# Performance work log

Measured on AMD Instinct MI355X. Metric: run time of the kernel, lower is better.

## Reference

```python
import jax, jax.numpy as jnp
import numpy as np

B, T = 128, 2048
O, E, L = 128, 512, 34  # o_size, embed_dim, num_letter


def setup_inputs() -> dict:
    key = jax.random.key(0)
    ks = jax.random.split(key, 16)
    u = lambda k, shape, s: jax.random.uniform(k, shape, jnp.float32, -s, s)
    hk = jax.random.normal(ks[0], (B, T, O), jnp.float32)
    hv = jax.random.normal(ks[1], (B, T, O), jnp.float32)
    y_1 = jax.random.normal(ks[2], (B, E), jnp.float32)
    c_1 = jax.random.normal(ks[3], (B, O), jnp.float32)
    sh_1 = jax.random.normal(ks[4], (B, O), jnp.float32)
    sc_1 = jax.random.normal(ks[5], (B, O), jnp.float32)
    # valid-length mask (each row has at least T//2 valid positions)
    lengths = jax.random.randint(ks[6], (B,), T // 2, T + 1)
    mask = (jnp.arange(T)[None, :] < lengths[:, None]).astype(jnp.float32)
    s_rnn = 1.0 / np.sqrt(O)
    W_ih = u(ks[7], (4 * O, O + E), s_rnn)
    b_ih = u(ks[8], (4 * O,), s_rnn)
    W_hh = u(ks[9], (4 * O, O), s_rnn)
    b_hh = u(ks[10], (4 * O,), s_rnn)
    s1 = 1.0 / np.sqrt(O)
    W1 = u(ks[11], (L, O), s1); b1 = u(ks[12], (L,), s1)
    W2 = u(ks[13], (L, O), s1); b2 = u(ks[14], (L,), s1)
    s3 = 1.0 / np.sqrt(L)
    W3 = u(ks[15], (L, L), s3); b3 = u(jax.random.fold_in(key, 99), (L,), s3)
    return {"hk": hk, "hv": hv, "y_1": y_1, "c_1": c_1, "sh_1": sh_1,
            "sc_1": sc_1, "mask": mask, "W_ih": W_ih, "b_ih": b_ih,
            "W_hh": W_hh, "b_hh": b_hh, "W1": W1, "b1": b1,
            "W2": W2, "b2": b2, "W3": W3, "b3": b3}


def reference(hk, hv, y_1, c_1, sh_1, sc_1, mask,
              W_ih, b_ih, W_hh, b_hh, W1, b1, W2, b2, W3, b3):
    # LSTMCell (PyTorch gate order: i, f, g, o)
    x = jnp.concatenate([y_1, c_1], axis=1)            # [B, O+E]
    gates = x @ W_ih.T + b_ih + sh_1 @ W_hh.T + b_hh   # [B, 4O]
    i, f, g, o = jnp.split(gates, 4, axis=1)
    sc = jax.nn.sigmoid(f) * sc_1 + jax.nn.sigmoid(i) * jnp.tanh(g)
    sh = jax.nn.sigmoid(o) * jnp.tanh(sc)
    # attention scores keyed on cell state sc (faithful to source)
    scores = jnp.einsum('bto,bo->bt', hk, sc)          # [B, T]
    attn = jax.nn.softmax(scores, axis=1) * mask
    attn = attn / jnp.sum(attn, axis=1, keepdims=True)
    c = jnp.einsum('bt,bto->bo', attn, hv)             # [B, O]
    out = jax.nn.relu(sh @ W1.T + b1 + c @ W2.T + b2)
    out = jax.nn.softmax(out @ W3.T + b3, axis=1)      # [B, L]
    return (out, c, sh, sc)
```

## Files before the change

kernel.cpp:

```cpp
#include <hip/hip_runtime.h>
#include <math.h>

#define BB 128
#define TT 2048
#define OO 128
#define EE 512
#define LL 34
#define XDIM 640
#define CHUNKS 16
#define CHUNK_LEN 128

__device__ __forceinline__ float sigmoidf_(float x) { return 1.0f / (1.0f + __expf(-x)); }

__global__ __launch_bounds__(256) void lstm_kernel(
    const float* __restrict__ y1, const float* __restrict__ c1,
    const float* __restrict__ sh1, const float* __restrict__ sc1,
    const float* __restrict__ Wih, const float* __restrict__ bih,
    const float* __restrict__ Whh, const float* __restrict__ bhh,
    float* __restrict__ out_sh, float* __restrict__ out_sc)
{
    __shared__ float xs[4][768];
    __shared__ float gbuf[4][4][16];
    const int tid = threadIdx.x;
    const int otile = blockIdx.x;
    const int qb = blockIdx.y * 4;

    for (int idx = tid; idx < 4 * 768; idx += 256) {
        int bi = idx / 768, k = idx - bi * 768;
        int b = qb + bi;
        float v;
        if (k < 512)      v = y1[b * EE + k];
        else if (k < 640) v = c1[b * OO + (k - 512)];
        else              v = sh1[b * OO + (k - 640)];
        xs[bi][k] = v;
    }
    __syncthreads();

    const int g = tid >> 6, l = tid & 63;
    #pragma unroll 2
    for (int i = 0; i < 16; ++i) {
        const int row = g * 128 + otile * 16 + i;
        const float* wr = Wih + (size_t)row * XDIM;
        float a0 = 0.f, a1 = 0.f, a2 = 0.f, a3 = 0.f;
        #pragma unroll
        for (int j = 0; j < 10; ++j) {
            float wv = wr[l + 64 * j];
            a0 += wv * xs[0][l + 64 * j];
            a1 += wv * xs[1][l + 64 * j];
            a2 += wv * xs[2][l + 64 * j];
            a3 += wv * xs[3][l + 64 * j];
        }
        const float* wh = Whh + (size_t)row * OO;
        #pragma unroll
        for (int j = 0; j < 2; ++j) {
            float wv = wh[l + 64 * j];
            a0 += wv * xs[0][640 + l + 64 * j];
            a1 += wv * xs[1][640 + l + 64 * j];
            a2 += wv * xs[2][640 + l + 64 * j];
            a3 += wv * xs[3][640 + l + 64 * j];
        }
        #pragma unroll
        for (int off = 32; off >= 1; off >>= 1) {
            a0 += __shfl_xor(a0, off);
            a1 += __shfl_xor(a1, off);
            a2 += __shfl_xor(a2, off);
            a3 += __shfl_xor(a3, off);
        }
        if (l == 0) {
            float bb = bih[row] + bhh[row];
            gbuf[g][0][i] = a0 + bb;
            gbuf[g][1][i] = a1 + bb;
            gbuf[g][2][i] = a2 + bb;
            gbuf[g][3][i] = a3 + bb;
        }
    }
    __syncthreads();

    if (tid < 64) {
        const int bi = tid >> 4, ol = tid & 15;
        const int b = qb + bi, o = otile * 16 + ol;
        float gi = gbuf[0][bi][ol], gf = gbuf[1][bi][ol];
        float gg = gbuf[2][bi][ol], go = gbuf[3][bi][ol];
        float sc = sigmoidf_(gf) * sc1[b * OO + o] + sigmoidf_(gi) * tanhf(gg);
        float sh = sigmoidf_(go) * tanhf(sc);
        out_sc[b * OO + o] = sc;
        out_sh[b * OO + o] = sh;
    }
}

__global__ __launch_bounds__(256) void scores_kernel(
    const float* __restrict__ hk, const float* __restrict__ mask,
    const float* __restrict__ sc, float* __restrict__ wbuf,
    float2* __restrict__ pbuf)
{
    const int b = blockIdx.y, chunk = blockIdx.x;
    const int tid = threadIdx.x;
    const int sg = tid >> 4, l = tid & 15;

    const float4 scA = *(const float4*)(sc + b * OO + l * 8);
    const float4 scB = *(const float4*)(sc + b * OO + l * 8 + 4);

    const int r0 = chunk * CHUNK_LEN + sg * 8;
    const float* mrow = mask + (size_t)b * TT + r0;
    const float* krow = hk + ((size_t)b * TT + r0) * OO;

    float s[8];
    bool val[8];
    #pragma unroll
    for (int i = 0; i < 8; ++i) {
        val[i] = (mrow[i] != 0.f);
        float4 a = make_float4(0.f, 0.f, 0.f, 0.f);
        float4 c2 = make_float4(0.f, 0.f, 0.f, 0.f);
        if (val[i]) {
            a  = *(const float4*)(krow + (size_t)i * OO + l * 8);
            c2 = *(const float4*)(krow + (size_t)i * OO + l * 8 + 4);
        }
        s[i] = a.x * scA.x + a.y * scA.y + a.z * scA.z + a.w * scA.w
             + c2.x * scB.x + c2.y * scB.y + c2.z * scB.z + c2.w * scB.w;
    }
    #pragma unroll
    for (int i = 0; i < 8; ++i) {
        s[i] += __shfl_xor(s[i], 8);
        s[i] += __shfl_xor(s[i], 4);
        s[i] += __shfl_xor(s[i], 2);
        s[i] += __shfl_xor(s[i], 1);
    }
    float msg = -INFINITY;
    #pragma unroll
    for (int i = 0; i < 8; ++i) if (val[i]) msg = fmaxf(msg, s[i]);

    __shared__ float sm[16], ssum[16];
    if (l == 0) sm[sg] = msg;
    __syncthreads();
    float mc = sm[0];
    #pragma unroll
    for (int i = 1; i < 16; ++i) mc = fmaxf(mc, sm[i]);

    float psum = 0.f;
    float e[8];
    #pragma unroll
    for (int i = 0; i < 8; ++i) {
        e[i] = val[i] ? __expf(s[i] - mc) : 0.f;
        psum += e[i];
    }
    if (l == 0) ssum[sg] = psum;
    float* wrow = wbuf + (size_t)b * TT + r0;
    #pragma unroll
    for (int i = 0; i < 8; ++i)
        if (l == i) wrow[i] = e[i];
    __syncthreads();
    if (tid == 0) {
        float S = 0.f;
        #pragma unroll
        for (int i = 0; i < 16; ++i) S += ssum[i];
        pbuf[(size_t)b * CHUNKS + chunk] = make_float2(mc, S);
    }
}

__global__ __launch_bounds__(256) void wsum_kernel(
    const float* __restrict__ hv, const float* __restrict__ wbuf,
    const float2* __restrict__ pbuf, float* __restrict__ ws_c)
{
    const int b = blockIdx.y, chunk = blockIdx.x;
    const int tid = threadIdx.x;
    __shared__ float marr[CHUNKS], Sarr[CHUNKS];
    __shared__ float wsh[CHUNK_LEN];
    __shared__ float pacc[8][128];

    if (tid < CHUNKS) {
        float2 p = pbuf[(size_t)b * CHUNKS + tid];
        marr[tid] = p.x;
        Sarr[tid] = p.y;
    }
    __syncthreads();
    float M = marr[0];
    #pragma unroll
    for (int i = 1; i < CHUNKS; ++i) M = fmaxf(M, marr[i]);
    float S = 0.f;
    #pragma unroll
    for (int i = 0; i < CHUNKS; ++i) S += Sarr[i] * __expf(marr[i] - M);
    const float factor = __expf(marr[chunk] - M) / S;

    if (tid < CHUNK_LEN)
        wsh[tid] = wbuf[(size_t)b * TT + chunk * CHUNK_LEN + tid] * factor;
    __syncthreads();

    const int o4 = tid & 31, rr = tid >> 5;
    const float* vbase = hv + ((size_t)b * TT + chunk * CHUNK_LEN) * OO + o4 * 4;
    float4 acc = make_float4(0.f, 0.f, 0.f, 0.f);
    #pragma unroll 8
    for (int j = 0; j < 16; ++j) {
        const int r = rr + 8 * j;
        const float wr = wsh[r];
        if (wr != 0.f) {
            float4 v = *(const float4*)(vbase + (size_t)r * OO);
            acc.x += wr * v.x;
            acc.y += wr * v.y;
            acc.z += wr * v.z;
            acc.w += wr * v.w;
        }
    }
    *(float4*)&pacc[rr][o4 * 4] = acc;
    __syncthreads();

    if (tid < 128) {
        float s = 0.f;
        #pragma unroll
        for (int i = 0; i < 8; ++i) s += pacc[i][tid];
        ws_c[((size_t)b * CHUNKS + chunk) * OO + tid] = s;
    }
}

__global__ __launch_bounds__(256) void final_kernel(
    const float* __restrict__ ws_c, const float* __restrict__ sh_in,
    const float* __restrict__ W1, const float* __restrict__ b1,
    const float* __restrict__ W2, const float* __restrict__ b2,
    const float* __restrict__ W3, const float* __restrict__ b3,
    float* __restrict__ out_p, float* __restrict__ out_c)
{
    const int b = blockIdx.x, tid = threadIdx.x;
    __shared__ float cbuf[128], shbuf[128], h1[LL], zz[LL], red2[2];

    if (tid < 128) {
        float s = 0.f;
        const float* base = ws_c + (size_t)b * CHUNKS * OO + tid;
        #pragma unroll
        for (int i = 0; i < CHUNKS; ++i) s += base[i * OO];
        cbuf[tid] = s;
        out_c[b * OO + tid] = s;
        shbuf[tid] = sh_in[b * OO + tid];
    }
    __syncthreads();

    const int o = tid >> 2, l2 = tid & 3;
    if (o < LL) {
        float a = 0.f;
        const float* w1r = W1 + o * OO;
        const float* w2r = W2 + o * OO;
        #pragma unroll 8
        for (int j = 0; j < 32; ++j) {
            int k = l2 + 4 * j;
            a += w1r[k] * shbuf[k] + w2r[k] * cbuf[k];
        }
        a += __shfl_xor(a, 1);
        a += __shfl_xor(a, 2);
        if (l2 == 0) h1[o] = fmaxf(a + b1[o] + b2[o], 0.f);
    }
    __syncthreads();

    if (o < LL) {
        float z = 0.f;
        const float* w3r = W3 + o * LL;
        for (int j = 0; j < 9; ++j) {
            int k = l2 + 4 * j;
            if (k < LL) z += w3r[k] * h1[k];
        }
        z += __shfl_xor(z, 1);
        z += __shfl_xor(z, 2);
        if (l2 == 0) zz[o] = z + b3[o];
    }
    __syncthreads();
    if (tid == 0) {
        float mm = zz[0];
        for (int i = 1; i < LL; i++) mm = fmaxf(mm, zz[i]);
        float ss = 0.f;
        for (int i = 0; i < LL; i++) ss += __expf(zz[i] - mm);
        red2[0] = mm; red2[1] = ss;
    }
    __syncthreads();
    if (tid < LL) out_p[b * LL + tid] = __expf(zz[tid] - red2[0]) / red2[1];
}

extern "C" void kernel_launch(void* const* d_in, const int* in_sizes, int n_in,
                              void* d_out, int out_size, void* d_ws, size_t ws_size,
                              hipStream_t stream) {
    (void)in_sizes; (void)n_in; (void)out_size; (void)ws_size;
    const float* hk   = (const float*)d_in[0];
    const float* hv   = (const float*)d_in[1];
    const float* y1   = (const float*)d_in[2];
    const float* c1   = (const float*)d_in[3];
    const float* sh1  = (const float*)d_in[4];
    const float* sc1  = (const float*)d_in[5];
    const float* mask = (const float*)d_in[6];
    const float* Wih  = (const float*)d_in[7];
    const float* bih  = (const float*)d_in[8];
    const float* Whh  = (const float*)d_in[9];
    const float* bhh  = (const float*)d_in[10];
    const float* W1   = (const float*)d_in[11];
    const float* b1   = (const float*)d_in[12];
    const float* W2   = (const float*)d_in[13];
    const float* b2   = (const float*)d_in[14];
    const float* W3   = (const float*)d_in[15];
    const float* b3   = (const float*)d_in[16];

    float* out    = (float*)d_out;
    float* out_c  = out + BB * LL;
    float* out_sh = out_c + BB * OO;
    float* out_sc = out_sh + BB * OO;

    float*  wbuf = (float*)d_ws;
    float*  ws_c = wbuf + (size_t)BB * TT;
    float2* pbuf = (float2*)(ws_c + (size_t)BB * CHUNKS * OO);

    lstm_kernel<<<dim3(8, 32), 256, 0, stream>>>(y1, c1, sh1, sc1, Wih, bih, Whh, bhh,
                                                 out_sh, out_sc);
    scores_kernel<<<dim3(CHUNKS, BB), 256, 0, stream>>>(hk, mask, out_sc, wbuf, pbuf);
    wsum_kernel<<<dim3(CHUNKS, BB), 256, 0, stream>>>(hv, wbuf, pbuf, ws_c);
    final_kernel<<<BB, 256, 0, stream>>>(ws_c, out_sh, W1, b1, W2, b2, W3, b3,
                                         out, out_c);
}
```

Before: 328.2 us.

## Fuse score and weighted-sum kernels with deferred per-chunk softmax rescaling

Merges the attention score kernel and the value-weighted-sum kernel into one kernel. Each chunk keeps unnormalized exponentials in shared memory and writes only its local max and sum. The final kernel rescales the per-chunk partial sums by the global max and normalizer. This removes one kernel launch and the global round trip of the weight buffer, in exchange for slightly more work in the final kernel and more shared memory per block.

```diff
diff --git a/kernel.cpp b/kernel.cpp
--- a/kernel.cpp
+++ b/kernel.cpp
@@ -88,15 +88,18 @@
     }
 }
 
-__global__ __launch_bounds__(256) void scores_kernel(
-    const float* __restrict__ hk, const float* __restrict__ mask,
-    const float* __restrict__ sc, float* __restrict__ wbuf,
-    float2* __restrict__ pbuf)
+__global__ __launch_bounds__(256) void attn_kernel(
+    const float* __restrict__ hk, const float* __restrict__ hv,
+    const float* __restrict__ mask, const float* __restrict__ sc,
+    float2* __restrict__ pbuf, float* __restrict__ ws_c)
 {
     const int b = blockIdx.y, chunk = blockIdx.x;
     const int tid = threadIdx.x;
+    __shared__ float sm[16], ssum[16];
+    __shared__ float wsh[CHUNK_LEN];
+    __shared__ float pacc[8][128];
+
     const int sg = tid >> 4, l = tid & 15;
-
     const float4 scA = *(const float4*)(sc + b * OO + l * 8);
     const float4 scB = *(const float4*)(sc + b * OO + l * 8 + 4);
 
@@ -128,8 +131,6 @@
     float msg = -INFINITY;
     #pragma unroll
     for (int i = 0; i < 8; ++i) if (val[i]) msg = fmaxf(msg, s[i]);
-
-    __shared__ float sm[16], ssum[16];
     if (l == 0) sm[sg] = msg;
     __syncthreads();
     float mc = sm[0];
@@ -137,17 +138,13 @@
     for (int i = 1; i < 16; ++i) mc = fmaxf(mc, sm[i]);
 
     float psum = 0.f;
-    float e[8];
     #pragma unroll
     for (int i = 0; i < 8; ++i) {
-        e[i] = val[i] ? __expf(s[i] - mc) : 0.f;
-        psum += e[i];
+        float e = val[i] ? __expf(s[i] - mc) : 0.f;
+        psum += e;
+        if (l == i) wsh[sg * 8 + i] = e;
     }
     if (l == 0) ssum[sg] = psum;
-    float* wrow = wbuf + (size_t)b * TT + r0;
-    #pragma unroll
-    for (int i = 0; i < 8; ++i)
-        if (l == i) wrow[i] = e[i];
     __syncthreads();
     if (tid == 0) {
         float S = 0.f;
@@ -155,35 +152,6 @@
         for (int i = 0; i < 16; ++i) S += ssum[i];
         pbuf[(size_t)b * CHUNKS + chunk] = make_float2(mc, S);
     }
-}
-
-__global__ __launch_bounds__(256) void wsum_kernel(
-    const float* __restrict__ hv, const float* __restrict__ wbuf,
-    const float2* __restrict__ pbuf, float* __restrict__ ws_c)
-{
-    const int b = blockIdx.y, chunk = blockIdx.x;
-    const int tid = threadIdx.x;
-    __shared__ float marr[CHUNKS], Sarr[CHUNKS];
-    __shared__ float wsh[CHUNK_LEN];
-    __shared__ float pacc[8][128];
-
-    if (tid < CHUNKS) {
-        float2 p = pbuf[(size_t)b * CHUNKS + tid];
-        marr[tid] = p.x;
-        Sarr[tid] = p.y;
-    }
-    __syncthreads();
-    float M = marr[0];
-    #pragma unroll
-    for (int i = 1; i < CHUNKS; ++i) M = fmaxf(M, marr[i]);
-    float S = 0.f;
-    #pragma unroll
-    for (int i = 0; i < CHUNKS; ++i) S += Sarr[i] * __expf(marr[i] - M);
-    const float factor = __expf(marr[chunk] - M) / S;
-
-    if (tid < CHUNK_LEN)
-        wsh[tid] = wbuf[(size_t)b * TT + chunk * CHUNK_LEN + tid] * factor;
-    __syncthreads();
 
     const int o4 = tid & 31, rr = tid >> 5;
     const float* vbase = hv + ((size_t)b * TT + chunk * CHUNK_LEN) * OO + o4 * 4;
@@ -204,28 +172,46 @@
     __syncthreads();
 
     if (tid < 128) {
-        float s = 0.f;
-        #pragma unroll
-        for (int i = 0; i < 8; ++i) s += pacc[i][tid];
-        ws_c[((size_t)b * CHUNKS + chunk) * OO + tid] = s;
+        float s2 = 0.f;
+        #pragma unroll
+        for (int i = 0; i < 8; ++i) s2 += pacc[i][tid];
+        ws_c[((size_t)b * CHUNKS + chunk) * OO + tid] = s2;
     }
 }
 
 __global__ __launch_bounds__(256) void final_kernel(
-    const float* __restrict__ ws_c, const float* __restrict__ sh_in,
+    const float2* __restrict__ pbuf, const float* __restrict__ ws_c,
+    const float* __restrict__ sh_in,
     const float* __restrict__ W1, const float* __restrict__ b1,
     const float* __restrict__ W2, const float* __restrict__ b2,
     const float* __restrict__ W3, const float* __restrict__ b3,
     float* __restrict__ out_p, float* __restrict__ out_c)
 {
     const int b = blockIdx.x, tid = threadIdx.x;
+    __shared__ float marr[CHUNKS], Sarr[CHUNKS];
     __shared__ float cbuf[128], shbuf[128], h1[LL], zz[LL], red2[2];
+
+    if (tid < CHUNKS) {
+        float2 p = pbuf[(size_t)b * CHUNKS + tid];
+        marr[tid] = p.x;
+        Sarr[tid] = p.y;
+    }
+    __syncthreads();
+    float M = marr[0];
+    #pragma unroll
+    for (int i = 1; i < CHUNKS; ++i) M = fmaxf(M, marr[i]);
+    float S = 0.f;
+    #pragma unroll
+    for (int i = 0; i < CHUNKS; ++i) S += Sarr[i] * __expf(marr[i] - M);
+    const float invS = 1.f / S;
 
     if (tid < 128) {
         float s = 0.f;
         const float* base = ws_c + (size_t)b * CHUNKS * OO + tid;
         #pragma unroll
-        for (int i = 0; i < CHUNKS; ++i) s += base[i * OO];
+        for (int i = 0; i < CHUNKS; ++i)
+            s += base[i * OO] * __expf(marr[i] - M);
+        s *= invS;
         cbuf[tid] = s;
         out_c[b * OO + tid] = s;
         shbuf[tid] = sh_in[b * OO + tid];
@@ -298,14 +284,12 @@
     float* out_sh = out_c + BB * OO;
     float* out_sc = out_sh + BB * OO;
 
-    float*  wbuf = (float*)d_ws;
-    float*  ws_c = wbuf + (size_t)BB * TT;
+    float*  ws_c = (float*)d_ws;
     float2* pbuf = (float2*)(ws_c + (size_t)BB * CHUNKS * OO);
 
     lstm_kernel<<<dim3(8, 32), 256, 0, stream>>>(y1, c1, sh1, sc1, Wih, bih, Whh, bhh,
                                                  out_sh, out_sc);
-    scores_kernel<<<dim3(CHUNKS, BB), 256, 0, stream>>>(hk, mask, out_sc, wbuf, pbuf);
-    wsum_kernel<<<dim3(CHUNKS, BB), 256, 0, stream>>>(hv, wbuf, pbuf, ws_c);
-    final_kernel<<<BB, 256, 0, stream>>>(ws_c, out_sh, W1, b1, W2, b2, W3, b3,
+    attn_kernel<<<dim3(CHUNKS, BB), 256, 0, stream>>>(hk, hv, mask, out_sc, pbuf, ws_c);
+    final_kernel<<<BB, 256, 0, stream>>>(pbuf, ws_c, out_sh, W1, b1, W2, b2, W3, b3,
                                          out, out_c);
 }
```

After: 329.1 us. No clear change (+0.3%).
